# Kernel optimization log

Hardware: AMD Instinct MI355X
Metric: run time of the kernel (lower is better)

Reference implementation:

```python
import jax, jax.numpy as jnp
import numpy as np

H = 768
NH = 12
HD = H // NH  # 64


def setup_inputs() -> dict:
    key = jax.random.key(0)
    ks = jax.random.split(key, 8)
    B, S = 4, 2048
    sc = 1.0 / np.sqrt(H)
    return {
        "hidden_states": jax.random.normal(ks[0], (B, S, H), dtype=jnp.float32),
        "attention_mask": jnp.zeros((B, 1, 1, S), dtype=jnp.float32),
        "Wq": jax.random.normal(ks[1], (H, H), dtype=jnp.float32) * sc,
        "bq": jnp.zeros((H,), dtype=jnp.float32),
        "Wk": jax.random.normal(ks[2], (H, H), dtype=jnp.float32) * sc,
        "bk": jnp.zeros((H,), dtype=jnp.float32),
        "Wv": jax.random.normal(ks[3], (H, H), dtype=jnp.float32) * sc,
        "bv": jnp.zeros((H,), dtype=jnp.float32),
    }


def _split_heads(x):
    # [B,S,H] -> [B,NH,S,HD]
    B, S, _ = x.shape
    return x.reshape(B, S, NH, HD).transpose(0, 2, 1, 3)


def reference(hidden_states, attention_mask, Wq, bq, Wk, bk, Wv, bv):
    q = _split_heads(hidden_states @ Wq + bq)
    k = _split_heads(hidden_states @ Wk + bk)
    v = _split_heads(hidden_states @ Wv + bv)
    # scores: [B,NH,S,S]
    scores = jnp.einsum("bhqd,bhkd->bhqk", q, k) / np.sqrt(HD)
    scores = scores + attention_mask
    probs = jax.nn.softmax(scores, axis=-1)  # dropout is identity in eval
    ctx = jnp.einsum("bhqk,bhkd->bhqd", probs, v)
    B, _, S, _ = ctx.shape
    return ctx.transpose(0, 2, 1, 3).reshape(B, S, H)
```

## Files before the change

kernel.cpp:

```cpp
#include <hip/hip_runtime.h>
#include <stdint.h>

typedef short bf16x8 __attribute__((ext_vector_type(8)));
typedef float f32x4  __attribute__((ext_vector_type(4)));
typedef float f32x16 __attribute__((ext_vector_type(16)));
typedef unsigned short u16;

#define B_  4
#define S_  2048
#define H_  768
#define NH_ 12
#define HD_ 64
#define NPROJ_N (3*H_)

static __device__ __forceinline__ u16 f2bf(float f) {
    union { float f; unsigned int u; } x; x.f = f;
    return (u16)((x.u + 0x8000u) >> 16);
}
static __device__ __forceinline__ bf16x8 ld8(const u16* p) {
    return *(const bf16x8*)(const void*)p;
}
static __device__ __forceinline__ void st8(u16* p, bf16x8 v) {
    *(bf16x8*)(void*)p = v;
}
static __device__ __forceinline__ void async_ld16(const u16* g, const short* l) {
    __builtin_amdgcn_global_load_lds(
        (__attribute__((address_space(1))) void*)g,
        (__attribute__((address_space(3))) void*)l,
        16, 0, 0);
}
static __device__ __forceinline__ unsigned cvtpk(float a, float b) {
    unsigned r;
    asm("v_cvt_pk_bf16_f32 %0, %1, %2" : "=v"(r) : "v"(a), "v"(b));
    return r;
}
static __device__ __forceinline__ void pl32swap(unsigned& a, unsigned& b) {
    asm("v_permlane32_swap_b32 %0, %1" : "+v"(a), "+v"(b));
}
static __device__ __forceinline__ bf16x8 mk8(unsigned a, unsigned b, unsigned c, unsigned d) {
    union { unsigned u[4]; bf16x8 v; } x;
    x.u[0] = a; x.u[1] = b; x.u[2] = c; x.u[3] = d;
    return x.v;
}

__global__ __launch_bounds__(256) void prep_kernel(const float* __restrict__ in,
                                                   u16* __restrict__ out,
                                                   const float* __restrict__ wq,
                                                   const float* __restrict__ wk,
                                                   const float* __restrict__ wv,
                                                   u16* __restrict__ wt,
                                                   const float* __restrict__ amask,
                                                   float* __restrict__ msc) {
    __shared__ float t[32][33];
    const int blk = blockIdx.x;
    const int tid = threadIdx.x;
    if (blk < 6144) {
        int i = (blk * 256 + tid) * 4;
        float4 v = *(const float4*)(in + i);
        ushort4 o;
        o.x = f2bf(v.x); o.y = f2bf(v.y); o.z = f2bf(v.z); o.w = f2bf(v.w);
        *(ushort4*)(out + i) = o;
    } else if (blk < 7872) {
        const int idx  = blk - 6144;
        const int proj = idx / 576;
        const int rem  = idx % 576;
        const int bx = rem % 24, by = rem / 24;
        const float* w = (proj == 0) ? wq : (proj == 1) ? wk : wv;
        u16* o = wt + (size_t)proj * H_ * H_;
        const int tx = tid & 31, ty = tid >> 5;
        const int n0 = bx * 32, k0 = by * 32;
        #pragma unroll
        for (int i = 0; i < 4; i++)
            t[ty + i * 8][tx] = w[(size_t)(k0 + ty + i * 8) * H_ + n0 + tx];
        __syncthreads();
        #pragma unroll
        for (int i = 0; i < 4; i++)
            o[(size_t)(n0 + ty + i * 8) * H_ + k0 + tx] = f2bf(t[tx][ty + i * 8]);
    } else {
        const int i = ((blk - 7872) * 256 + tid) * 8;
        float4 a0 = *(const float4*)(amask + i);
        float4 a1 = *(const float4*)(amask + i + 4);
        a0.x *= 1.44269504f; a0.y *= 1.44269504f; a0.z *= 1.44269504f; a0.w *= 1.44269504f;
        a1.x *= 1.44269504f; a1.y *= 1.44269504f; a1.z *= 1.44269504f; a1.w *= 1.44269504f;
        *(float4*)(msc + i)     = a0;
        *(float4*)(msc + i + 4) = a1;
    }
}

__global__ __launch_bounds__(256) void qkv_gemm(const u16* __restrict__ A,
                                                const u16* __restrict__ Wt,
                                                const float* __restrict__ bq,
                                                const float* __restrict__ bk,
                                                const float* __restrict__ bv,
                                                u16* __restrict__ qo,
                                                u16* __restrict__ ko,
                                                u16* __restrict__ vto) {
    __shared__ alignas(16) short SMEM[4][128 * 64];

    const int tid  = threadIdx.x;
    const int wave = tid >> 6;
    const int lane = tid & 63;
    const int quad = lane >> 4;
    const int l16  = lane & 15;
    const int wm   = wave & 1;
    const int wn   = wave >> 1;

    const int id  = blockIdx.x;
    const int xcd = id & 7;
    const int j   = id >> 3;
    const int mi  = j & 7;
    const int ni  = j >> 3;
    const int m0 = (xcd * 8 + mi) * 128;
    const int n0 = ni * 128;

    int stR[4], stC[4];
    #pragma unroll
    for (int jj = 0; jj < 4; jj++) {
        const int lc = wave * 256 + jj * 64 + lane;
        stR[jj] = lc >> 3;
        stC[jj] = ((lc & 7) ^ (stR[jj] & 7)) * 8;
    }
    const int fx0 = (quad ^ (l16 & 7)) * 8;
    const int fx1 = fx0 ^ 32;

    f32x4 acc[4][4];
    #pragma unroll
    for (int i = 0; i < 4; i++)
        #pragma unroll
        for (int jj = 0; jj < 4; jj++) acc[i][jj] = (f32x4)0.0f;

#define GSTAGE(kt_, buf_)                                                                     \
    do {                                                                                      \
        const int kk_ = (kt_) * 64;                                                           \
        _Pragma("unroll")                                                                     \
        for (int jj = 0; jj < 4; jj++) {                                                      \
            async_ld16(A  + (size_t)(m0 + stR[jj]) * H_ + kk_ + stC[jj],                      \
                       &SMEM[(buf_) * 2][(wave * 256 + jj * 64) * 8]);                        \
            async_ld16(Wt + (size_t)(n0 + stR[jj]) * H_ + kk_ + stC[jj],                      \
                       &SMEM[(buf_) * 2 + 1][(wave * 256 + jj * 64) * 8]);                    \
        }                                                                                     \
    } while (0)

    GSTAGE(0, 0);
    __syncthreads();

    for (int kt = 0; kt < 12; kt++) {
        const int cur = kt & 1;
        if (kt + 1 < 12) GSTAGE(kt + 1, cur ^ 1);
        const short* As = SMEM[cur * 2];
        const short* Bs = SMEM[cur * 2 + 1];
        #pragma unroll
        for (int ks = 0; ks < 2; ks++) {
            const int fx = ks ? fx1 : fx0;
            bf16x8 af[4], bfr[4];
            #pragma unroll
            for (int i = 0; i < 4; i++)
                af[i] = *(const bf16x8*)(const void*)&As[(wm * 64 + i * 16 + l16) * 64 + fx];
            #pragma unroll
            for (int jj = 0; jj < 4; jj++)
                bfr[jj] = *(const bf16x8*)(const void*)&Bs[(wn * 64 + jj * 16 + l16) * 64 + fx];
            #pragma unroll
            for (int i = 0; i < 4; i++)
                #pragma unroll
                for (int jj = 0; jj < 4; jj++)
                    acc[i][jj] = __builtin_amdgcn_mfma_f32_16x16x32_bf16(af[i], bfr[jj], acc[i][jj], 0, 0, 0);
        }
        __syncthreads();
    }
#undef GSTAGE

    const int proj  = n0 / H_;
    const int hbase = (n0 % H_) >> 6;
    const float* bias = (proj == 0) ? bq : (proj == 1) ? bk : bv;
    u16* Ct = (u16*)SMEM;

    #pragma unroll
    for (int nj = 0; nj < 4; nj++) {
        const int nl = wn * 64 + nj * 16 + l16;
        const float bv_ = bias[(n0 % H_) + nl];
        #pragma unroll
        for (int mi2 = 0; mi2 < 4; mi2++) {
            #pragma unroll
            for (int r = 0; r < 4; r++) {
                const int ml = wm * 64 + mi2 * 16 + quad * 4 + r;
                const u16 val = f2bf(acc[mi2][nj][r] + bv_);
                if (proj < 2)
                    Ct[ml * 128 + ((nl + (ml & 15) * 8) & 127)] = val;
                else
                    Ct[nl * 128 + ((ml + (nl & 15) * 8) & 127)] = val;
            }
        }
    }
    __syncthreads();

    if (proj < 2) {
        u16* dst0 = (proj == 0) ? qo : ko;
        const int c = tid & 7;
        #pragma unroll
        for (int jj = 0; jj < 8; jj++) {
            const int idx = jj * 32 + (tid >> 3);
            const int ml = idx >> 1, h2 = idx & 1;
            const int nbase = h2 * 64 + c * 8;
            bf16x8 v8 = *(const bf16x8*)(const void*)&Ct[ml * 128 + ((nbase + (ml & 15) * 8) & 127)];
            const int m = m0 + ml;
            const int b = m >> 11, s = m & 2047;
            st8(dst0 + ((size_t)(b * NH_ + hbase + h2) * S_ + s) * HD_ + c * 8, v8);
        }
    } else {
        const int b = m0 >> 11;
        #pragma unroll
        for (int jj = 0; jj < 8; jj++) {
            const int nl = (tid >> 3) + (jj & 3) * 32;
            const int c  = (tid & 7) + (jj >> 2) * 8;
            bf16x8 v8 = *(const bf16x8*)(const void*)&Ct[nl * 128 + ((c * 8 + (nl & 15) * 8) & 127)];
            const int h2 = nl >> 6, d = nl & 63;
            st8(vto + ((size_t)(b * NH_ + hbase + h2) * HD_ + d) * S_ + (m0 & 2047) + c * 8, v8);
        }
    }
}

__global__ __launch_bounds__(256, 3) void attn_kernel(const u16* __restrict__ q,
                                                      const u16* __restrict__ k,
                                                      const u16* __restrict__ vt,
                                                      const float* __restrict__ msc,
                                                      float* __restrict__ out) {
    __shared__ alignas(16) short Ks[2][64 * 64];
    __shared__ alignas(16) short Vs[2][64 * 64];

    const int tid  = threadIdx.x;
    const int wave = tid >> 6;
    const int lane = tid & 63;
    const int l32  = lane & 31;
    const int h    = lane >> 5;

    const int bh = blockIdx.x;
    const int b  = bh / NH_;
    const int q0 = blockIdx.y * 128;
    const float C1 = 0.125f * 1.44269504f;

    const u16* qrow = q + ((size_t)bh * S_ + q0 + wave * 32 + l32) * HD_;
    bf16x8 qf[4];
    #pragma unroll
    for (int i = 0; i < 4; i++) qf[i] = ld8(qrow + i * 16 + h * 8);

    const u16* kbase = k  + (size_t)bh * S_ * HD_;
    const u16* vbase = vt + (size_t)bh * HD_ * S_;
    const float* mrow = msc + (size_t)b * S_ + h * 4;

    const int sRow = tid >> 3;
    const int sCol = ((tid & 7) ^ (sRow & 7)) * 8;
    const int rx   = l32 & 7;

    union { unsigned u[4]; bf16x8 v; } one_;
    one_.u[0] = 0x3F803F80u; one_.u[1] = 0x3F803F80u;
    one_.u[2] = 0x3F803F80u; one_.u[3] = 0x3F803F80u;
    const bf16x8 ones = one_.v;

    f32x16 lsacc = (f32x16)0.0f;
    f32x16 oacc0 = (f32x16)0.0f;
    f32x16 oacc1 = (f32x16)0.0f;

#define STAGE(kt_, buf_)                                                                           \
    do {                                                                                           \
        async_ld16(kbase + (size_t)(kt_) * 4096 + sRow * 64 + sCol,          &Ks[buf_][tid * 8]);  \
        async_ld16(kbase + (size_t)(kt_) * 4096 + (sRow + 32) * 64 + sCol,   &Ks[buf_][2048 + tid * 8]); \
        async_ld16(vbase + (size_t)sRow * S_ + (kt_) * 64 + sCol,            &Vs[buf_][tid * 8]);  \
        async_ld16(vbase + (size_t)(sRow + 32) * S_ + (kt_) * 64 + sCol,     &Vs[buf_][2048 + tid * 8]); \
    } while (0)

    STAGE(0, 0);
    __syncthreads();

    for (int kt = 0; kt < S_ / 64; kt++) {
        const int cur = kt & 1;

        const float* mb = mrow + kt * 64;
        f32x4 mm0[4], mm1[4];
        #pragma unroll
        for (int c = 0; c < 4; c++) {
            mm0[c] = *(const f32x4*)(mb + c * 8);
            mm1[c] = *(const f32x4*)(mb + 32 + c * 8);
        }

        if (kt + 1 < S_ / 64) STAGE(kt + 1, cur ^ 1);
        const short* Kc = Ks[cur];
        const short* Vc = Vs[cur];

        f32x16 s0 = (f32x16)0.0f;
        f32x16 s1 = (f32x16)0.0f;
        __builtin_amdgcn_s_setprio(1);
        #pragma unroll
        for (int i = 0; i < 4; i++) {
            const int ch = ((h + 2 * i) ^ rx) * 8;
            bf16x8 kf0 = *(const bf16x8*)(const void*)&Kc[l32 * 64 + ch];
            bf16x8 kf1 = *(const bf16x8*)(const void*)&Kc[(l32 + 32) * 64 + ch];
            s0 = __builtin_amdgcn_mfma_f32_32x32x16_bf16(kf0, qf[i], s0, 0, 0, 0);
            s1 = __builtin_amdgcn_mfma_f32_32x32x16_bf16(kf1, qf[i], s1, 0, 0, 0);
        }
        __builtin_amdgcn_s_setprio(0);

        unsigned w0[8], w1[8];
        #pragma unroll
        for (int c = 0; c < 4; c++) {
            const float p00 = __builtin_amdgcn_exp2f(__builtin_fmaf(s0[4*c+0], C1, mm0[c][0]));
            const float p01 = __builtin_amdgcn_exp2f(__builtin_fmaf(s0[4*c+1], C1, mm0[c][1]));
            const float p02 = __builtin_amdgcn_exp2f(__builtin_fmaf(s0[4*c+2], C1, mm0[c][2]));
            const float p03 = __builtin_amdgcn_exp2f(__builtin_fmaf(s0[4*c+3], C1, mm0[c][3]));
            const float p10 = __builtin_amdgcn_exp2f(__builtin_fmaf(s1[4*c+0], C1, mm1[c][0]));
            const float p11 = __builtin_amdgcn_exp2f(__builtin_fmaf(s1[4*c+1], C1, mm1[c][1]));
            const float p12 = __builtin_amdgcn_exp2f(__builtin_fmaf(s1[4*c+2], C1, mm1[c][2]));
            const float p13 = __builtin_amdgcn_exp2f(__builtin_fmaf(s1[4*c+3], C1, mm1[c][3]));
            w0[2*c]   = cvtpk(p00, p01);
            w0[2*c+1] = cvtpk(p02, p03);
            w1[2*c]   = cvtpk(p10, p11);
            w1[2*c+1] = cvtpk(p12, p13);
        }

        bf16x8 pa[4];
        #pragma unroll
        for (int t = 0; t < 2; t++) {
            {
                unsigned a = w0[4*t+0], bb = w0[4*t+2];
                pl32swap(a, bb);
                unsigned c2 = w0[4*t+1], dd = w0[4*t+3];
                pl32swap(c2, dd);
                pa[t] = mk8(a, c2, bb, dd);
            }
            {
                unsigned a = w1[4*t+0], bb = w1[4*t+2];
                pl32swap(a, bb);
                unsigned c2 = w1[4*t+1], dd = w1[4*t+3];
                pl32swap(c2, dd);
                pa[2 + t] = mk8(a, c2, bb, dd);
            }
        }

        __builtin_amdgcn_s_setprio(1);
        #pragma unroll
        for (int t = 0; t < 4; t++) {
            const int ch = ((h + 2 * t) ^ rx) * 8;
            bf16x8 vf0 = *(const bf16x8*)(const void*)&Vc[l32 * 64 + ch];
            bf16x8 vf1 = *(const bf16x8*)(const void*)&Vc[(l32 + 32) * 64 + ch];
            oacc0 = __builtin_amdgcn_mfma_f32_32x32x16_bf16(pa[t], vf0, oacc0, 0, 0, 0);
            oacc1 = __builtin_amdgcn_mfma_f32_32x32x16_bf16(pa[t], vf1, oacc1, 0, 0, 0);
            lsacc = __builtin_amdgcn_mfma_f32_32x32x16_bf16(pa[t], ones, lsacc, 0, 0, 0);
        }
        __builtin_amdgcn_s_setprio(0);
        __syncthreads();
    }
#undef STAGE

    const int hh = bh % NH_;
    #pragma unroll
    for (int r = 0; r < 16; r++) {
        const int qq = (r & 3) + 8 * (r >> 2) + 4 * h;
        const float linv = 1.0f / lsacc[r];
        const int s = q0 + wave * 32 + qq;
        float* orow = out + ((size_t)b * S_ + s) * H_ + hh * 64 + l32;
        orow[0]  = oacc0[r] * linv;
        orow[32] = oacc1[r] * linv;
    }
}

extern "C" void kernel_launch(void* const* d_in, const int* in_sizes, int n_in,
                              void* d_out, int out_size, void* d_ws, size_t ws_size,
                              hipStream_t stream) {
    const float* hidden = (const float*)d_in[0];
    const float* amask  = (const float*)d_in[1];
    const float* Wq     = (const float*)d_in[2];
    const float* bq     = (const float*)d_in[3];
    const float* Wk     = (const float*)d_in[4];
    const float* bk     = (const float*)d_in[5];
    const float* Wv     = (const float*)d_in[6];
    const float* bv     = (const float*)d_in[7];
    float* out = (float*)d_out;

    char* ws = (char*)d_ws;
    const size_t sz_hidden = (size_t)B_ * S_ * H_ * 2;
    const size_t sz_wt     = (size_t)NPROJ_N * H_ * 2;
    const size_t sz_qkv    = (size_t)B_ * S_ * H_ * 2;

    u16* hid_bf = (u16*)(ws);
    u16* wt     = (u16*)(ws + sz_hidden);
    u16* qbuf   = (u16*)(ws + sz_hidden + sz_wt);
    u16* kbuf   = (u16*)(ws + sz_hidden + sz_wt + sz_qkv);
    u16* vtbuf  = (u16*)(ws + sz_hidden + sz_wt + 2 * sz_qkv);
    float* msc  = (float*)(ws + sz_hidden + sz_wt + 3 * sz_qkv);

    prep_kernel<<<dim3(6144 + 1728 + 4), dim3(256), 0, stream>>>(
        hidden, hid_bf, Wq, Wk, Wv, wt, amask, msc);
    qkv_gemm<<<dim3(1152), dim3(256), 0, stream>>>(
        hid_bf, wt, bq, bk, bv, qbuf, kbuf, vtbuf);
    attn_kernel<<<dim3(B_ * NH_, S_ / 128), dim3(256), 0, stream>>>(
        qbuf, kbuf, vtbuf, msc, out);
}
```

Baseline: 213.1 us.

## Split key tile across wave pairs and compute row sums on VALU

Each wave now handles 64 query rows against half of every 64-key tile instead of 32 rows against the whole tile, so one K fragment load feeds two MFMAs and V fragments are reused across two query blocks. The ones-matrix MFMA for row sums is replaced by scalar accumulation of the probabilities, and the mask row is staged once into shared memory rather than reloaded from global memory each iteration. Partial outputs and sums from the two key-half waves are combined through shared memory at the end. This costs extra accumulator registers, 8KB more LDS and a final cross-wave reduction, which may lower occupancy. Row sums are now taken from the fp32 probabilities rather than their bf16-rounded values.

```diff
diff --git a/kernel.cpp b/kernel.cpp
--- a/kernel.cpp
+++ b/kernel.cpp
@@ -224,41 +224,52 @@
                                                       const u16* __restrict__ vt,
                                                       const float* __restrict__ msc,
                                                       float* __restrict__ out) {
-    __shared__ alignas(16) short Ks[2][64 * 64];
-    __shared__ alignas(16) short Vs[2][64 * 64];
+    __shared__ alignas(16) short Ks[2][4096];
+    __shared__ alignas(16) short Vs[2][4096];
+    __shared__ alignas(16) float Ms[S_];
 
     const int tid  = threadIdx.x;
     const int wave = tid >> 6;
     const int lane = tid & 63;
     const int l32  = lane & 31;
     const int h    = lane >> 5;
+    const int kh   = wave & 1;
+    const int qg   = wave >> 1;
 
     const int bh = blockIdx.x;
     const int b  = bh / NH_;
     const int q0 = blockIdx.y * 128;
     const float C1 = 0.125f * 1.44269504f;
 
-    const u16* qrow = q + ((size_t)bh * S_ + q0 + wave * 32 + l32) * HD_;
-    bf16x8 qf[4];
+    {
+        const float* mrow = msc + (size_t)b * S_;
+        float4 a0 = *(const float4*)(mrow + tid * 8);
+        float4 a1 = *(const float4*)(mrow + tid * 8 + 4);
+        *(float4*)(Ms + tid * 8)     = a0;
+        *(float4*)(Ms + tid * 8 + 4) = a1;
+    }
+
+    bf16x8 qf[2][4];
     #pragma unroll
-    for (int i = 0; i < 4; i++) qf[i] = ld8(qrow + i * 16 + h * 8);
+    for (int qb = 0; qb < 2; qb++) {
+        const u16* qrow = q + ((size_t)bh * S_ + q0 + qg * 64 + qb * 32 + l32) * HD_;
+        #pragma unroll
+        for (int i = 0; i < 4; i++) qf[qb][i] = ld8(qrow + i * 16 + h * 8);
+    }
 
     const u16* kbase = k  + (size_t)bh * S_ * HD_;
     const u16* vbase = vt + (size_t)bh * HD_ * S_;
-    const float* mrow = msc + (size_t)b * S_ + h * 4;
 
     const int sRow = tid >> 3;
     const int sCol = ((tid & 7) ^ (sRow & 7)) * 8;
     const int rx   = l32 & 7;
 
-    union { unsigned u[4]; bf16x8 v; } one_;
-    one_.u[0] = 0x3F803F80u; one_.u[1] = 0x3F803F80u;
-    one_.u[2] = 0x3F803F80u; one_.u[3] = 0x3F803F80u;
-    const bf16x8 ones = one_.v;
-
-    f32x16 lsacc = (f32x16)0.0f;
-    f32x16 oacc0 = (f32x16)0.0f;
-    f32x16 oacc1 = (f32x16)0.0f;
+    float ls0 = 0.f, ls1 = 0.f;
+    f32x16 oacc[2][2];
+    #pragma unroll
+    for (int qb = 0; qb < 2; qb++)
+        #pragma unroll
+        for (int dh = 0; dh < 2; dh++) oacc[qb][dh] = (f32x16)0.0f;
 
 #define STAGE(kt_, buf_)                                                                           \
     do {                                                                                           \
@@ -273,15 +284,6 @@
 
     for (int kt = 0; kt < S_ / 64; kt++) {
         const int cur = kt & 1;
-
-        const float* mb = mrow + kt * 64;
-        f32x4 mm0[4], mm1[4];
-        #pragma unroll
-        for (int c = 0; c < 4; c++) {
-            mm0[c] = *(const f32x4*)(mb + c * 8);
-            mm1[c] = *(const f32x4*)(mb + 32 + c * 8);
-        }
-
         if (kt + 1 < S_ / 64) STAGE(kt + 1, cur ^ 1);
         const short* Kc = Ks[cur];
         const short* Vc = Vs[cur];
@@ -291,32 +293,33 @@
         __builtin_amdgcn_s_setprio(1);
         #pragma unroll
         for (int i = 0; i < 4; i++) {
-            const int ch = ((h + 2 * i) ^ rx) * 8;
-            bf16x8 kf0 = *(const bf16x8*)(const void*)&Kc[l32 * 64 + ch];
-            bf16x8 kf1 = *(const bf16x8*)(const void*)&Kc[(l32 + 32) * 64 + ch];
-            s0 = __builtin_amdgcn_mfma_f32_32x32x16_bf16(kf0, qf[i], s0, 0, 0, 0);
-            s1 = __builtin_amdgcn_mfma_f32_32x32x16_bf16(kf1, qf[i], s1, 0, 0, 0);
+            bf16x8 kf = *(const bf16x8*)(const void*)&Kc[kh * 2048 + l32 * 64 + (((h + 2 * i) ^ rx) * 8)];
+            s0 = __builtin_amdgcn_mfma_f32_32x32x16_bf16(kf, qf[0][i], s0, 0, 0, 0);
+            s1 = __builtin_amdgcn_mfma_f32_32x32x16_bf16(kf, qf[1][i], s1, 0, 0, 0);
         }
         __builtin_amdgcn_s_setprio(0);
 
         unsigned w0[8], w1[8];
         #pragma unroll
         for (int c = 0; c < 4; c++) {
-            const float p00 = __builtin_amdgcn_exp2f(__builtin_fmaf(s0[4*c+0], C1, mm0[c][0]));
-            const float p01 = __builtin_amdgcn_exp2f(__builtin_fmaf(s0[4*c+1], C1, mm0[c][1]));
-            const float p02 = __builtin_amdgcn_exp2f(__builtin_fmaf(s0[4*c+2], C1, mm0[c][2]));
-            const float p03 = __builtin_amdgcn_exp2f(__builtin_fmaf(s0[4*c+3], C1, mm0[c][3]));
-            const float p10 = __builtin_amdgcn_exp2f(__builtin_fmaf(s1[4*c+0], C1, mm1[c][0]));
-            const float p11 = __builtin_amdgcn_exp2f(__builtin_fmaf(s1[4*c+1], C1, mm1[c][1]));
-            const float p12 = __builtin_amdgcn_exp2f(__builtin_fmaf(s1[4*c+2], C1, mm1[c][2]));
-            const float p13 = __builtin_amdgcn_exp2f(__builtin_fmaf(s1[4*c+3], C1, mm1[c][3]));
+            const f32x4 mm = *(const f32x4*)&Ms[kt * 64 + kh * 32 + c * 8 + h * 4];
+            const float p00 = __builtin_amdgcn_exp2f(__builtin_fmaf(s0[4*c+0], C1, mm[0]));
+            const float p01 = __builtin_amdgcn_exp2f(__builtin_fmaf(s0[4*c+1], C1, mm[1]));
+            const float p02 = __builtin_amdgcn_exp2f(__builtin_fmaf(s0[4*c+2], C1, mm[2]));
+            const float p03 = __builtin_amdgcn_exp2f(__builtin_fmaf(s0[4*c+3], C1, mm[3]));
+            const float p10 = __builtin_amdgcn_exp2f(__builtin_fmaf(s1[4*c+0], C1, mm[0]));
+            const float p11 = __builtin_amdgcn_exp2f(__builtin_fmaf(s1[4*c+1], C1, mm[1]));
+            const float p12 = __builtin_amdgcn_exp2f(__builtin_fmaf(s1[4*c+2], C1, mm[2]));
+            const float p13 = __builtin_amdgcn_exp2f(__builtin_fmaf(s1[4*c+3], C1, mm[3]));
             w0[2*c]   = cvtpk(p00, p01);
             w0[2*c+1] = cvtpk(p02, p03);
             w1[2*c]   = cvtpk(p10, p11);
             w1[2*c+1] = cvtpk(p12, p13);
-        }
-
-        bf16x8 pa[4];
+            ls0 += (p00 + p01) + (p02 + p03);
+            ls1 += (p10 + p11) + (p12 + p13);
+        }
+
+        bf16x8 pa0[2], pa1[2];
         #pragma unroll
         for (int t = 0; t < 2; t++) {
             {
@@ -324,41 +327,73 @@
                 pl32swap(a, bb);
                 unsigned c2 = w0[4*t+1], dd = w0[4*t+3];
                 pl32swap(c2, dd);
-                pa[t] = mk8(a, c2, bb, dd);
+                pa0[t] = mk8(a, c2, bb, dd);
             }
             {
                 unsigned a = w1[4*t+0], bb = w1[4*t+2];
                 pl32swap(a, bb);
                 unsigned c2 = w1[4*t+1], dd = w1[4*t+3];
                 pl32swap(c2, dd);
-                pa[2 + t] = mk8(a, c2, bb, dd);
+                pa1[t] = mk8(a, c2, bb, dd);
             }
         }
 
         __builtin_amdgcn_s_setprio(1);
         #pragma unroll
-        for (int t = 0; t < 4; t++) {
-            const int ch = ((h + 2 * t) ^ rx) * 8;
-            bf16x8 vf0 = *(const bf16x8*)(const void*)&Vc[l32 * 64 + ch];
-            bf16x8 vf1 = *(const bf16x8*)(const void*)&Vc[(l32 + 32) * 64 + ch];
-            oacc0 = __builtin_amdgcn_mfma_f32_32x32x16_bf16(pa[t], vf0, oacc0, 0, 0, 0);
-            oacc1 = __builtin_amdgcn_mfma_f32_32x32x16_bf16(pa[t], vf1, oacc1, 0, 0, 0);
-            lsacc = __builtin_amdgcn_mfma_f32_32x32x16_bf16(pa[t], ones, lsacc, 0, 0, 0);
+        for (int t = 0; t < 2; t++) {
+            #pragma unroll
+            for (int dh = 0; dh < 2; dh++) {
+                bf16x8 vf = *(const bf16x8*)(const void*)&Vc[dh * 2048 + l32 * 64 + (((kh * 4 + 2 * t + h) ^ rx) * 8)];
+                oacc[0][dh] = __builtin_amdgcn_mfma_f32_32x32x16_bf16(pa0[t], vf, oacc[0][dh], 0, 0, 0);
+                oacc[1][dh] = __builtin_amdgcn_mfma_f32_32x32x16_bf16(pa1[t], vf, oacc[1][dh], 0, 0, 0);
+            }
         }
         __builtin_amdgcn_s_setprio(0);
         __syncthreads();
     }
 #undef STAGE
 
-    const int hh = bh % NH_;
-    #pragma unroll
-    for (int r = 0; r < 16; r++) {
-        const int qq = (r & 3) + 8 * (r >> 2) + 4 * h;
-        const float linv = 1.0f / lsacc[r];
-        const int s = q0 + wave * 32 + qq;
-        float* orow = out + ((size_t)b * S_ + s) * H_ + hh * 64 + l32;
-        orow[0]  = oacc0[r] * linv;
-        orow[32] = oacc1[r] * linv;
+    ls0 += __shfl_xor(ls0, 32);
+    ls1 += __shfl_xor(ls1, 32);
+
+    float* R = qg ? (float*)Vs : (float*)Ks;
+
+    if (kh == 1) {
+        #pragma unroll
+        for (int qb = 0; qb < 2; qb++)
+            #pragma unroll
+            for (int dh = 0; dh < 2; dh++)
+                #pragma unroll
+                for (int r = 0; r < 16; r++) {
+                    const int qrow = (r & 3) + 8 * (r >> 2) + 4 * h;
+                    R[(qb * 32 + qrow) * 64 + dh * 32 + l32] = oacc[qb][dh][r];
+                }
+        if (lane < 32) {
+            Ms[qg * 64 + l32]      = ls0;
+            Ms[qg * 64 + 32 + l32] = ls1;
+        }
+    }
+    __syncthreads();
+
+    if (kh == 0) {
+        const float li0 = 1.0f / (ls0 + Ms[qg * 64 + l32]);
+        const float li1 = 1.0f / (ls1 + Ms[qg * 64 + 32 + l32]);
+        const int hh = bh % NH_;
+        #pragma unroll
+        for (int r = 0; r < 16; r++) {
+            const int qrow = (r & 3) + 8 * (r >> 2) + 4 * h;
+            const float lv0 = __shfl(li0, qrow);
+            const float lv1 = __shfl(li1, qrow);
+            #pragma unroll
+            for (int dh = 0; dh < 2; dh++) {
+                const int d = dh * 32 + l32;
+                const int s0r = q0 + qg * 64 + qrow;
+                out[((size_t)b * S_ + s0r) * H_ + hh * 64 + d] =
+                    (oacc[0][dh][r] + R[qrow * 64 + d]) * lv0;
+                out[((size_t)b * S_ + s0r + 32) * H_ + hh * 64 + d] =
+                    (oacc[1][dh][r] + R[(32 + qrow) * 64 + d]) * lv1;
+            }
+        }
     }
 }
 
```

Measured after the change: 204.2 us. -4.2%, faster.
